# Kernel optimization log

Measured on AMD Instinct MI355X. Metric: run time of the kernel, lower is better.

## Reference

```python
import jax, jax.numpy as jnp
import numpy as np

VOXEL_SIZE = (0.1, 0.1, 0.2)
PC_RANGE = (-51.2, -51.2, -5.0, 51.2, 51.2, 3.0)
B, N, C = 8, 1_000_000, 4


def setup_inputs() -> dict:
    key = jax.random.key(0)
    u = jax.random.uniform(key, (B, N, C), dtype=jnp.float32)
    # xyz spread slightly beyond the point-cloud range so some points are out-of-range;
    # 4th channel is an intensity in [0, 1].
    lo = jnp.array([-60.0, -60.0, -8.0, 0.0], jnp.float32)
    hi = jnp.array([60.0, 60.0, 6.0, 1.0], jnp.float32)
    pts = lo + u * (hi - lo)
    # inject NaNs to exercise the not_nan_mask path
    pts = pts.at[:, ::1000, 0].set(jnp.nan)
    return {"points": pts}


def reference(points):
    # Padded/masked equivalent of DynamicVoxelizer.forward.
    # Instead of stream-compacting each batch (dynamic shapes), we return
    # fixed-shape [B, N, ...] arrays plus a validity mask; invalid entries
    # carry the same sentinel (-1 coords / -1 idx) the torch code filters on.
    vs = jnp.array(VOXEL_SIZE, dtype=points.dtype)          # (3,) x,y,z
    rng = jnp.array(PC_RANGE, dtype=points.dtype)           # (6,)
    pmin = rng[:3]
    grid = jnp.round((rng[3:] - rng[:3]) / vs).astype(jnp.int32)  # (nx, ny, nz)

    xyz = points[..., :3]                                   # [B, N, 3]
    not_nan = ~jnp.isnan(points).any(axis=-1)               # [B, N]

    # dynamic voxelization (mmcv semantics, max_num_points=-1):
    # per-point integer voxel coordinate, -1 sentinel if out of grid.
    cf = jnp.floor((xyz - pmin) / vs)                       # [B, N, 3] float (x,y,z order)
    c = cf.astype(jnp.int32)
    in_range = ((c >= 0) & (c < grid)).all(axis=-1)         # [B, N]
    valid = not_nan & in_range                              # [B, N]

    # voxelizer returns coords in (z, y, x) order; -1 where invalid
    voxel_coords = jnp.where(valid[..., None], c[..., ::-1], -1)

    # _get_point_offsets: reorder zyx->xyz, center = coord*vs + min + vs/2
    centers = cf * vs + pmin + vs * 0.5                     # [B, N, 3]
    point_offsets = jnp.where(valid[..., None], xyz - centers, 0.0)

    point_idxes = jnp.where(valid, jnp.arange(N, dtype=jnp.int32)[None, :], -1)
    points_out = jnp.where(valid[..., None], points, 0.0)

    return points_out, voxel_coords, point_idxes, point_offsets, valid
```

## Files before the change

kernel.cpp:

```cpp
#include <hip/hip_runtime.h>


#define NPTS 1000000

struct F3 { float x, y, z; };

__global__ __launch_bounds__(256) void voxelize_kernel(
    const float4* __restrict__ pts, float* __restrict__ out, int total) {
  int i = blockIdx.x * blockDim.x + threadIdx.x;
  if (i >= total) return;

  float4 p = pts[i];

  bool has_nan = (p.x != p.x) | (p.y != p.y) | (p.z != p.z) | (p.w != p.w);

  float fx = floorf((p.x - (-51.2f)) / 0.1f);
  float fy = floorf((p.y - (-51.2f)) / 0.1f);
  float fz = floorf((p.z - (-5.0f))  / 0.2f);
  int cx = (int)fx, cy = (int)fy, cz = (int)fz;

  bool in_range = (cx >= 0) & (cx < 1024) &
                  (cy >= 0) & (cy < 1024) &
                  (cz >= 0) & (cz < 40);
  bool valid = (!has_nan) && in_range;

  float ox = p.x - (fx * 0.1f + (-51.2f) + 0.05f);
  float oy = p.y - (fy * 0.1f + (-51.2f) + 0.05f);
  float oz = p.z - (fz * 0.2f + (-5.0f)  + 0.1f);

  long long t = total;
  float*  pout = out;
  F3*     vox  = (F3*)(out + 4 * t);
  float*  idx  = out + 7 * t;
  F3*     poff = (F3*)(out + 8 * t);
  float*  pval = out + 11 * t;

  float4 po;
  if (valid) { po = p; } else { po.x = po.y = po.z = po.w = 0.0f; }
  ((float4*)pout)[i] = po;

  F3 vc, of;
  if (valid) {
    vc.x = (float)cz; vc.y = (float)cy; vc.z = (float)cx;
    of.x = ox; of.y = oy; of.z = oz;
  } else {
    vc.x = vc.y = vc.z = -1.0f;
    of.x = of.y = of.z = 0.0f;
  }
  vox[i]  = vc;
  poff[i] = of;

  idx[i]  = valid ? (float)(i % NPTS) : -1.0f;
  pval[i] = valid ? 1.0f : 0.0f;
}

extern "C" void kernel_launch(void* const* d_in, const int* in_sizes, int n_in,
                              void* d_out, int out_size, void* d_ws, size_t ws_size,
                              hipStream_t stream) {
  (void)n_in; (void)d_ws; (void)ws_size; (void)out_size;
  const float4* pts = (const float4*)d_in[0];
  float* out = (float*)d_out;
  int total = in_sizes[0] / 4;
  int block = 256;
  int grid = (total + block - 1) / block;
  voxelize_kernel<<<grid, block, 0, stream>>>(pts, out, total);
}
```

Before: 456.8 us.

## Stage strided outputs through LDS for coalesced 16-byte nontemporal stores

The per-thread 12-byte voxel-coord and offset writes and the scalar idx/valid writes are now staged in shared memory, then written back by the block as aligned 16-byte vector stores. All global loads and stores use nontemporal hints so the streaming traffic does not pollute cache. A separate tail kernel handles leftover points that do not fill a full block. This adds a block barrier and some LDS traffic per block.

```diff
diff --git a/kernel.cpp b/kernel.cpp
--- a/kernel.cpp
+++ b/kernel.cpp
@@ -2,15 +2,21 @@
 
 
 #define NPTS 1000000
+#define BLK 256
 
-struct F3 { float x, y, z; };
+typedef float f4 __attribute__((ext_vector_type(4)));
 
-__global__ __launch_bounds__(256) void voxelize_kernel(
-    const float4* __restrict__ pts, float* __restrict__ out, int total) {
-  int i = blockIdx.x * blockDim.x + threadIdx.x;
-  if (i >= total) return;
+__global__ __launch_bounds__(BLK) void voxelize_kernel(
+    const f4* __restrict__ pts, float* __restrict__ out, int total) {
+  __shared__ __align__(16) float s_vox[BLK * 3];
+  __shared__ __align__(16) float s_poff[BLK * 3];
+  __shared__ __align__(16) float s_misc[BLK * 2];
 
-  float4 p = pts[i];
+  const int tid  = threadIdx.x;
+  const int base = blockIdx.x * BLK;
+  const int i    = base + tid;
+
+  f4 p = __builtin_nontemporal_load(&pts[i]);
 
   bool has_nan = (p.x != p.x) | (p.y != p.y) | (p.z != p.z) | (p.w != p.w);
 
@@ -28,40 +34,99 @@
   float oy = p.y - (fy * 0.1f + (-51.2f) + 0.05f);
   float oz = p.z - (fz * 0.2f + (-5.0f)  + 0.1f);
 
+  f4 po = valid ? p : (f4){0.0f, 0.0f, 0.0f, 0.0f};
+  __builtin_nontemporal_store(po, &((f4*)out)[i]);
+
+  if (valid) {
+    s_vox[tid * 3 + 0] = (float)cz;
+    s_vox[tid * 3 + 1] = (float)cy;
+    s_vox[tid * 3 + 2] = (float)cx;
+    s_poff[tid * 3 + 0] = ox;
+    s_poff[tid * 3 + 1] = oy;
+    s_poff[tid * 3 + 2] = oz;
+    s_misc[tid]       = (float)(i % NPTS);
+    s_misc[BLK + tid] = 1.0f;
+  } else {
+    s_vox[tid * 3 + 0] = -1.0f;
+    s_vox[tid * 3 + 1] = -1.0f;
+    s_vox[tid * 3 + 2] = -1.0f;
+    s_poff[tid * 3 + 0] = 0.0f;
+    s_poff[tid * 3 + 1] = 0.0f;
+    s_poff[tid * 3 + 2] = 0.0f;
+    s_misc[tid]       = -1.0f;
+    s_misc[BLK + tid] = 0.0f;
+  }
+  __syncthreads();
+
+  const long long t = total;
+  f4* gvox  = (f4*)(out + 4 * t  + (long long)base * 3);
+  f4* gpoff = (f4*)(out + 8 * t  + (long long)base * 3);
+  f4* gidx  = (f4*)(out + 7 * t  + base);
+  f4* gval  = (f4*)(out + 11 * t + base);
+
+  const f4* v4 = (const f4*)s_vox;
+  const f4* o4 = (const f4*)s_poff;
+  const f4* m4 = (const f4*)s_misc;
+
+  if (tid < 192) {
+    __builtin_nontemporal_store(v4[tid], &gvox[tid]);
+    __builtin_nontemporal_store(o4[tid], &gpoff[tid]);
+  } else {
+    int j = tid - 192;
+    __builtin_nontemporal_store(m4[j],      &gidx[j]);
+    __builtin_nontemporal_store(m4[64 + j], &gval[j]);
+  }
+}
+
+__global__ __launch_bounds__(64) void voxelize_tail(
+    const float* __restrict__ ptsf, float* __restrict__ out, int total, int start) {
+  int i = start + blockIdx.x * blockDim.x + threadIdx.x;
+  if (i >= total) return;
+  float px = ptsf[i * 4 + 0], py = ptsf[i * 4 + 1];
+  float pz = ptsf[i * 4 + 2], pw = ptsf[i * 4 + 3];
+  bool has_nan = (px != px) | (py != py) | (pz != pz) | (pw != pw);
+  float fx = floorf((px - (-51.2f)) / 0.1f);
+  float fy = floorf((py - (-51.2f)) / 0.1f);
+  float fz = floorf((pz - (-5.0f))  / 0.2f);
+  int cx = (int)fx, cy = (int)fy, cz = (int)fz;
+  bool in_range = (cx >= 0) & (cx < 1024) & (cy >= 0) & (cy < 1024) &
+                  (cz >= 0) & (cz < 40);
+  bool valid = (!has_nan) && in_range;
+  float ox = px - (fx * 0.1f + (-51.2f) + 0.05f);
+  float oy = py - (fy * 0.1f + (-51.2f) + 0.05f);
+  float oz = pz - (fz * 0.2f + (-5.0f)  + 0.1f);
   long long t = total;
-  float*  pout = out;
-  F3*     vox  = (F3*)(out + 4 * t);
-  float*  idx  = out + 7 * t;
-  F3*     poff = (F3*)(out + 8 * t);
-  float*  pval = out + 11 * t;
-
-  float4 po;
-  if (valid) { po = p; } else { po.x = po.y = po.z = po.w = 0.0f; }
-  ((float4*)pout)[i] = po;
-
-  F3 vc, of;
+  out[i * 4 + 0] = valid ? px : 0.0f;
+  out[i * 4 + 1] = valid ? py : 0.0f;
+  out[i * 4 + 2] = valid ? pz : 0.0f;
+  out[i * 4 + 3] = valid ? pw : 0.0f;
+  float* vox  = out + 4 * t  + (long long)i * 3;
+  float* poff = out + 8 * t  + (long long)i * 3;
   if (valid) {
-    vc.x = (float)cz; vc.y = (float)cy; vc.z = (float)cx;
-    of.x = ox; of.y = oy; of.z = oz;
+    vox[0] = (float)cz; vox[1] = (float)cy; vox[2] = (float)cx;
+    poff[0] = ox; poff[1] = oy; poff[2] = oz;
+    out[7 * t + i]  = (float)(i % NPTS);
+    out[11 * t + i] = 1.0f;
   } else {
-    vc.x = vc.y = vc.z = -1.0f;
-    of.x = of.y = of.z = 0.0f;
+    vox[0] = -1.0f; vox[1] = -1.0f; vox[2] = -1.0f;
+    poff[0] = 0.0f; poff[1] = 0.0f; poff[2] = 0.0f;
+    out[7 * t + i]  = -1.0f;
+    out[11 * t + i] = 0.0f;
   }
-  vox[i]  = vc;
-  poff[i] = of;
-
-  idx[i]  = valid ? (float)(i % NPTS) : -1.0f;
-  pval[i] = valid ? 1.0f : 0.0f;
 }
 
 extern "C" void kernel_launch(void* const* d_in, const int* in_sizes, int n_in,
                               void* d_out, int out_size, void* d_ws, size_t ws_size,
                               hipStream_t stream) {
   (void)n_in; (void)d_ws; (void)ws_size; (void)out_size;
-  const float4* pts = (const float4*)d_in[0];
+  const f4* pts = (const f4*)d_in[0];
   float* out = (float*)d_out;
   int total = in_sizes[0] / 4;
-  int block = 256;
-  int grid = (total + block - 1) / block;
-  voxelize_kernel<<<grid, block, 0, stream>>>(pts, out, total);
+  int full_blocks = total / BLK;
+  if (full_blocks > 0)
+    voxelize_kernel<<<full_blocks, BLK, 0, stream>>>(pts, out, total);
+  int rem = total - full_blocks * BLK;
+  if (rem > 0)
+    voxelize_tail<<<(rem + 63) / 64, 64, 0, stream>>>((const float*)d_in[0], out,
+                                                      total, full_blocks * BLK);
 }
```

New measurement: 443.5 us. -2.9%, faster.
